# Kernel tuning notes

Measured on AMD Instinct MI355X. Metric: run time of the kernel, lower is better.

The kernel has to match this reference:

```python
import jax, jax.numpy as jnp
import numpy as np


def lstm_cell(x, h, c, Wi, Wh, b):
    # PyTorch LSTMCell gate order: i, f, g, o
    g = x @ Wi.T + h @ Wh.T + b
    i, f, gg, o = jnp.split(g, 4, axis=-1)
    c = jax.nn.sigmoid(f) * c + jax.nn.sigmoid(i) * jnp.tanh(gg)
    h = jax.nn.sigmoid(o) * jnp.tanh(c)
    return h, c


def setup_inputs() -> dict:
    key = jax.random.key(0)
    ks = jax.random.split(key, 32)
    S, B, L, N, T = 20, 16, 30, 6, 20
    H, E, Vs, Vt = 512, 512, 50000, 30000
    w = lambda k, shape: jax.random.normal(k, shape, jnp.float32) * 0.05
    return {
        'articles': jax.random.randint(ks[0], (S, B, L), 0, Vs, jnp.int32),
        'summaries': jax.random.randint(ks[1], (N, B, T), 0, Vt, jnp.int32),
        'emb_src': w(ks[2], (Vs, E)),
        'emb_tgt': w(ks[3], (Vt, E)),
        'we_Wi': w(ks[4], (4 * H, E)), 'we_Wh': w(ks[5], (4 * H, H)), 'we_b': w(ks[6], (4 * H,)),
        'se_Wi': w(ks[7], (4 * H, H)), 'se_Wh': w(ks[8], (4 * H, H)), 'se_b': w(ks[9], (4 * H,)),
        'W_feat': w(ks[10], (H, H)), 'b_feat': w(ks[11], (H,)),
        'wd_Wi': w(ks[12], (4 * H, E)), 'wd_Wh': w(ks[13], (4 * H, H)), 'wd_b': w(ks[14], (4 * H,)),
        'W_vocab': w(ks[15], (Vt, H)), 'b_vocab': w(ks[16], (Vt,)),
        'sd_Wi': w(ks[17], (4 * H, H)), 'sd_Wh': w(ks[18], (4 * H, H)), 'sd_b': w(ks[19], (4 * H,)),
        'attn_Wh': w(ks[20], (H, H)), 'attn_wc': w(ks[21], (H,)), 'attn_v': w(ks[22], (H,)),
        'W_out': w(ks[23], (H, 2 * H)), 'b_out': w(ks[24], (H,)),
    }


def _forward(articles, summaries, emb_src, emb_tgt, we_Wi, we_Wh, we_b,
             se_Wi, se_Wh, se_b, W_feat, b_feat, wd_Wi, wd_Wh, wd_b,
             W_vocab, b_vocab, sd_Wi, sd_Wh, sd_b, attn_Wh, attn_wc, attn_v,
             W_out, b_out):
    S, B, L = articles.shape
    H = we_Wh.shape[1]

    # ---- word encoder: LSTMCell over each sentence, vmapped over S ----
    def encode_sentence(tokens):  # [B, L]
        x = emb_src[tokens]  # [B, L, E]
        z = jnp.zeros((B, H), x.dtype)
        def step(hc, xt):
            h, c = lstm_cell(xt, hc[0], hc[1], we_Wi, we_Wh, we_b)
            return (h, c), None
        (h, _), _ = jax.lax.scan(step, (z, z), jnp.swapaxes(x, 0, 1))
        return h
    word_hx = jax.vmap(encode_sentence)(articles)  # [S, B, H]

    # ---- sentence encoder: LSTM over sentence dim ----
    z = jnp.zeros((B, H), word_hx.dtype)
    def senc_step(hc, x):
        h, c = lstm_cell(x, hc[0], hc[1], se_Wi, se_Wh, se_b)
        return (h, c), h
    (s_hx, s_cx), sent_out = jax.lax.scan(senc_step, (z, z), word_hx)  # sent_out [S,B,H]
    sent_feat = sent_out @ W_feat.T + b_feat  # precomputed attention features

    mask = (articles[:, :, 0:1] > 0).astype(jnp.float32)  # [S, B, 1]
    coverage0 = jnp.zeros_like(mask)

    # ---- hierarchical decoder over summary sentences ----
    def sent_step(carry, sent):  # sent [B, T]
        w_hx, w_cx, s_hx, s_cx, coverage, loss = carry
        seq = sent.T  # [T, B]

        def word_step(wc, ba):
            wh, wcell, l = wc
            wb, wa = ba
            wh, wcell = lstm_cell(emb_tgt[wb], wh, wcell, wd_Wi, wd_Wh, wd_b)
            logits = wh @ W_vocab.T + b_vocab  # [B, V]
            logp = jax.nn.log_softmax(logits, axis=-1)
            nll = -jnp.take_along_axis(logp, wa[:, None], axis=1)[:, 0]
            m = (wa != 0).astype(logits.dtype)  # ignore_index=0
            l = l + jnp.sum(nll * m) / jnp.maximum(jnp.sum(m), 1.0)
            return (wh, wcell, l), None

        (w_hx, w_cx, loss), _ = jax.lax.scan(word_step, (w_hx, w_cx, loss), (seq[:-1], seq[1:]))

        # sentence decoder step with coverage attention over S sentences
        s_h2, s_cx = lstm_cell(w_hx, s_hx, s_cx, sd_Wi, sd_Wh, sd_b)
        e = jnp.einsum('sbh,h->sb', jnp.tanh(sent_feat + s_h2 @ attn_Wh.T + coverage * attn_wc), attn_v)
        e = jnp.where(mask[:, :, 0] > 0, e, -1e9)
        align = jax.nn.softmax(e, axis=0)[:, :, None]  # [S, B, 1]
        context = jnp.sum(align * sent_out, axis=0)  # [B, H]
        final = jnp.tanh(jnp.concatenate([context, s_h2], axis=-1) @ W_out.T + b_out)
        # coverage loss (with pre-update coverage), then accumulate coverage
        loss = loss + jnp.mean(jnp.sum(jnp.minimum(align[:, :, 0], coverage[:, :, 0]), axis=0))
        coverage = coverage + align
        return (final, w_cx, final, s_cx, coverage, loss), None

    init = (s_hx, s_cx, s_hx, s_cx, coverage0, jnp.float32(0.0))
    (_, _, _, _, _, loss), _ = jax.lax.scan(sent_step, init, summaries)
    return loss


def reference(articles, summaries, emb_src, emb_tgt, we_Wi, we_Wh, we_b,
              se_Wi, se_Wh, se_b, W_feat, b_feat, wd_Wi, wd_Wh, wd_b,
              W_vocab, b_vocab, sd_Wi, sd_Wh, sd_b, attn_Wh, attn_wc, attn_v,
              W_out, b_out):
    return _forward(articles, summaries, emb_src, emb_tgt, we_Wi, we_Wh, we_b,
                    se_Wi, se_Wh, se_b, W_feat, b_feat, wd_Wi, wd_Wh, wd_b,
                    W_vocab, b_vocab, sd_Wi, sd_Wh, sd_b, attn_Wh, attn_wc,
                    attn_v, W_out, b_out)
```

## Files before the change

kernel.cpp:

```cpp
#include <hip/hip_runtime.h>
#include <hip/hip_cooperative_groups.h>
#include <cstdint>
#include <cstddef>

namespace cg = cooperative_groups;

#define H 512
#define SS 20
#define BB 16
#define LL 30
#define NN 6
#define TT 20
#define VT 30000
#define MROWS 1824
#define NSTEPS 114
#define MPAD 1856
#define NT2 118
#define NVBLK 3422

typedef __attribute__((ext_vector_type(8))) short bf16x8;
typedef __attribute__((ext_vector_type(4))) float f32x4;

__device__ __forceinline__ float sigmoidf_(float x) { return 1.f / (1.f + expf(-x)); }
__device__ __forceinline__ float b2f(ushort u) { return __uint_as_float(((uint32_t)u) << 16); }
__device__ __forceinline__ ushort f2b_rne(float f) {
  uint32_t u = __float_as_uint(f);
  return (ushort)((u + 0x7fffu + ((u >> 16) & 1u)) >> 16);
}

struct PrepP {
  const int* articles; const int* summaries;
  const float* emb_src; const float* emb_tgt;
  const float* we_Wi; const float* wd_Wi; const float* we_Wh;
  const float* se_Wi; const float* se_Wh; const float* W_feat;
  const float* wd_Wh; const float* sd_Wi; const float* sd_Wh;
  const float* attn_Wh; const float* W_out;
  ushort* A_we; ushort* A_wd;
  ushort* weWi; ushort* wdWi; ushort* weWh;
  ushort* seWi; ushort* seWh; ushort* wfeat;
  ushort* wdWh; ushort* sdWi; ushort* sdWh;
  ushort* attnWh; ushort* Wout;
};

__device__ __forceinline__ void conv_f2b(const float* __restrict__ src,
                                         ushort* __restrict__ dst, int n4,
                                         int t0, int stride)
{
  for (int i = t0; i < n4; i += stride) {
    float4 v = reinterpret_cast<const float4*>(src)[i];
    ushort4 o;
    o.x = f2b_rne(v.x); o.y = f2b_rne(v.y);
    o.z = f2b_rne(v.z); o.w = f2b_rne(v.w);
    reinterpret_cast<ushort4*>(dst)[i] = o;
  }
}

__global__ __launch_bounds__(256) void prep_kernel(PrepP P)
{
  const int t0 = blockIdx.x * 256 + threadIdx.x;
  const int stride = gridDim.x * 256;
  for (int i = t0; i < SS * BB * LL * H; i += stride) {
    int m = i >> 9, k = i & 511;
    int l = m / (SS * BB), sb = m % (SS * BB);
    int tok = P.articles[sb * LL + l];
    P.A_we[i] = f2b_rne(P.emb_src[(size_t)tok * H + k]);
  }
  for (int i = t0; i < MROWS * H; i += stride) {
    int m = i >> 9, k = i & 511;
    int stp = m >> 4, b = m & 15;
    int n = stp / (TT - 1), t = stp % (TT - 1);
    int tok = P.summaries[(n * BB + b) * TT + t];
    P.A_wd[i] = f2b_rne(P.emb_tgt[(size_t)tok * H + k]);
  }
  const int Q = 4 * H * H / 4;
  conv_f2b(P.we_Wi, P.weWi, Q, t0, stride);
  conv_f2b(P.wd_Wi, P.wdWi, Q, t0, stride);
  conv_f2b(P.we_Wh, P.weWh, Q, t0, stride);
  conv_f2b(P.se_Wi, P.seWi, Q, t0, stride);
  conv_f2b(P.se_Wh, P.seWh, Q, t0, stride);
  conv_f2b(P.wd_Wh, P.wdWh, Q, t0, stride);
  conv_f2b(P.sd_Wi, P.sdWi, Q, t0, stride);
  conv_f2b(P.sd_Wh, P.sdWh, Q, t0, stride);
  conv_f2b(P.W_feat, P.wfeat, H * H / 4, t0, stride);
  conv_f2b(P.attn_Wh, P.attnWh, H * H / 4, t0, stride);
  conv_f2b(P.W_out, P.Wout, H * 2 * H / 4, t0, stride);
}

__global__ __launch_bounds__(512) void proj_mfma_kernel(
    const ushort* __restrict__ A_we, const ushort* __restrict__ weWi,
    const float* __restrict__ we_b, ushort* __restrict__ XiW,
    const ushort* __restrict__ A_wd, const ushort* __restrict__ wdWi,
    const float* __restrict__ wd_b, ushort* __restrict__ XiD)
{
  int bid = blockIdx.x;
  const ushort* A; const ushort* W; const float* bias; ushort* C; int M, mt, nt;
  if (bid < 1200) { A = A_we; W = weWi; bias = we_b; C = XiW; M = 9600; mt = bid >> 3; nt = bid & 7; }
  else { int b2 = bid - 1200; A = A_wd; W = wdWi; bias = wd_b; C = XiD; M = MROWS; mt = b2 >> 3; nt = b2 & 7; }
  const int tid = threadIdx.x, wid = tid >> 6, lane = tid & 63;
  const int wm = wid >> 2, wn = wid & 3;
  const int m0 = mt * 64 + wm * 32, n0 = nt * 256 + wn * 64;
  const int lr = lane & 15, lk = (lane >> 4) << 3;

  f32x4 acc[2][4];
#pragma unroll
  for (int i = 0; i < 2; ++i)
#pragma unroll
    for (int nf = 0; nf < 4; ++nf) acc[i][nf] = (f32x4)0.0f;

  for (int k0 = 0; k0 < H; k0 += 32) {
    bf16x8 a[2], b[4];
#pragma unroll
    for (int i = 0; i < 2; ++i) {
      int m = m0 + i * 16 + lr;
      bf16x8 az = (bf16x8)(short)0;
      if (m < M) az = *reinterpret_cast<const bf16x8*>(A + (size_t)m * H + k0 + lk);
      a[i] = az;
    }
#pragma unroll
    for (int nf = 0; nf < 4; ++nf)
      b[nf] = *reinterpret_cast<const bf16x8*>(W + (size_t)(n0 + nf * 16 + lr) * H + k0 + lk);
#pragma unroll
    for (int i = 0; i < 2; ++i)
#pragma unroll
      for (int nf = 0; nf < 4; ++nf)
        acc[i][nf] = __builtin_amdgcn_mfma_f32_16x16x32_bf16(a[i], b[nf], acc[i][nf], 0, 0, 0);
  }
#pragma unroll
  for (int i = 0; i < 2; ++i)
#pragma unroll
    for (int nf = 0; nf < 4; ++nf) {
      int n = n0 + nf * 16 + lr;
      float bv = bias[n];
#pragma unroll
      for (int jreg = 0; jreg < 4; ++jreg) {
        int row = m0 + i * 16 + (lane >> 4) * 4 + jreg;
        if (row < M) C[(size_t)row * 2048 + n] = f2b_rne(acc[i][nf][jreg] + bv);
      }
    }
}

struct UP {
  const ushort* XiW; const ushort* XiD;
  const ushort* weWh; const ushort* seWi; const ushort* seWh;
  const ushort* wfeat; const ushort* wdWh; const ushort* sdWi;
  const ushort* sdWh; const ushort* attnWh; const ushort* Wout;
  const float* se_b; const float* b_feat; const float* sd_b; const float* b_out;
  const float* attn_wc; const float* attn_v; const int* articles;
  ushort* h0; ushort* h1;
  float* XiS;
  ushort* sh0; ushort* sh1;
  float* sent_out;
  ushort* sent_out_bf;
  float* sent_feat;
  ushort* wh_bf;
  ushort* sdh_bf;
  ushort* final_bf;
  ushort* catb;
  float* qb;
  float* ebuf; float* alignb; float* covb; float* loss;
  const float* Wv; ushort* Wv_bf;
};

__global__ __launch_bounds__(512) void uni_kernel(UP P)
{
  cg::grid_group gg = cg::this_grid();
  const int tid = threadIdx.x, bid = blockIdx.x;
  const int wid = tid >> 6, lane = tid & 63;
  const int gw = bid * 8 + wid;
  const int lr = lane & 15;
  const int lk = (lane >> 4) << 3;
  const int orow = (lane >> 4) << 2;

  {
    float cst[5][4];
#pragma unroll
    for (int it = 0; it < 5; ++it)
#pragma unroll
      for (int rg = 0; rg < 4; ++rg) cst[it][rg] = 0.f;
    ushort* cur = P.h0;
    ushort* nxt = P.h1;
    const int ug = gw & 31;
    const int unit = ug * 16 + lr;
    const ushort* wb = P.weWh + (size_t)(ug * 16 + lr) * H + lk;
    for (int l = 0; l < LL; ++l) {
#pragma unroll
      for (int it = 0; it < 5; ++it) {
        int item = gw + it * 128;
        int mt = item >> 5;
        f32x4 acc[4];
#pragma unroll
        for (int g = 0; g < 4; ++g) acc[g] = (f32x4)0.0f;
        const ushort* ab = cur + (size_t)(mt * 16 + lr) * H + lk;
#pragma unroll
        for (int k0 = 0; k0 < H; k0 += 32) {
          bf16x8 a = *reinterpret_cast<const bf16x8*>(ab + k0);
#pragma unroll
          for (int g = 0; g < 4; ++g) {
            bf16x8 b = *reinterpret_cast<const bf16x8*>(wb + (size_t)g * H * H + k0);
            acc[g] = __builtin_amdgcn_mfma_f32_16x16x32_bf16(a, b, acc[g], 0, 0, 0);
          }
        }
#pragma unroll
        for (int rg = 0; rg < 4; ++rg) {
          int row = mt * 16 + orow + rg;
          const ushort* xi = P.XiW + (size_t)(l * 320 + row) * 2048 + unit;
          float gi = acc[0][rg] + b2f(xi[0]);
          float gf = acc[1][rg] + b2f(xi[512]);
          float gc = acc[2][rg] + b2f(xi[1024]);
          float go = acc[3][rg] + b2f(xi[1536]);
          float c = sigmoidf_(gf) * cst[it][rg] + sigmoidf_(gi) * tanhf(gc);
          float h = sigmoidf_(go) * tanhf(c);
          cst[it][rg] = c;
          nxt[(size_t)row * H + unit] = f2b_rne(h);
        }
      }
      gg.sync();
      ushort* t = cur; cur = nxt; nxt = t;
    }
    {
      const ushort* wbs = P.seWi + (size_t)(ug * 16 + lr) * H + lk;
#pragma unroll
      for (int it = 0; it < 5; ++it) {
        int item = gw + it * 128;
        int mt = item >> 5;
        f32x4 acc[4];
#pragma unroll
        for (int g = 0; g < 4; ++g) acc[g] = (f32x4)0.0f;
        const ushort* ab = cur + (size_t)(mt * 16 + lr) * H + lk;
#pragma unroll
        for (int k0 = 0; k0 < H; k0 += 32) {
          bf16x8 a = *reinterpret_cast<const bf16x8*>(ab + k0);
#pragma unroll
          for (int g = 0; g < 4; ++g) {
            bf16x8 b = *reinterpret_cast<const bf16x8*>(wbs + (size_t)g * H * H + k0);
            acc[g] = __builtin_amdgcn_mfma_f32_16x16x32_bf16(a, b, acc[g], 0, 0, 0);
          }
        }
#pragma unroll
        for (int rg = 0; rg < 4; ++rg) {
          int row = mt * 16 + orow + rg;
#pragma unroll
          for (int g = 0; g < 4; ++g)
            P.XiS[(size_t)row * 2048 + g * H + unit] = acc[g][rg] + P.se_b[g * H + unit];
        }
      }
    }
    {
      const int t0 = bid * 512 + tid;
      const int n4 = VT * H / 4;
      for (int i = t0; i < n4; i += 16 * 512) {
        float4 v = reinterpret_cast<const float4*>(P.Wv)[i];
        ushort4 o;
        o.x = f2b_rne(v.x); o.y = f2b_rne(v.y);
        o.z = f2b_rne(v.z); o.w = f2b_rne(v.w);
        reinterpret_cast<ushort4*>(P.Wv_bf)[i] = o;
      }
    }
    gg.sync();
  }

  float cw[4], csd[4];
  {
    float cse[4] = {0.f, 0.f, 0.f, 0.f};
    ushort* cur = P.sh0;
    ushort* nxt = P.sh1;
    const int ug = bid * 2 + wid;
    const int unit = ug * 16 + lr;
    for (int s = 0; s < SS; ++s) {
      if (wid < 2) {
        f32x4 acc[4];
#pragma unroll
        for (int g = 0; g < 4; ++g) acc[g] = (f32x4)0.0f;
        const ushort* ab = cur + (size_t)lr * H + lk;
        const ushort* wb = P.seWh + (size_t)(ug * 16 + lr) * H + lk;
#pragma unroll
        for (int k0 = 0; k0 < H; k0 += 32) {
          bf16x8 a = *reinterpret_cast<const bf16x8*>(ab + k0);
#pragma unroll
          for (int g = 0; g < 4; ++g) {
            bf16x8 b = *reinterpret_cast<const bf16x8*>(wb + (size_t)g * H * H + k0);
            acc[g] = __builtin_amdgcn_mfma_f32_16x16x32_bf16(a, b, acc[g], 0, 0, 0);
          }
        }
#pragma unroll
        for (int rg = 0; rg < 4; ++rg) {
          int row = orow + rg;
          const float* xi = P.XiS + (size_t)(s * 16 + row) * 2048 + unit;
          float gi = acc[0][rg] + xi[0];
          float gf = acc[1][rg] + xi[512];
          float gc = acc[2][rg] + xi[1024];
          float go = acc[3][rg] + xi[1536];
          float c = sigmoidf_(gf) * cse[rg] + sigmoidf_(gi) * tanhf(gc);
          float h = sigmoidf_(go) * tanhf(c);
          cse[rg] = c;
          nxt[(size_t)row * H + unit] = f2b_rne(h);
          P.sent_out[(size_t)(s * 16 + row) * H + unit] = h;
          P.sent_out_bf[(size_t)(s * 16 + row) * H + unit] = f2b_rne(h);
        }
      }
      gg.sync();
      ushort* t = cur; cur = nxt; nxt = t;
    }
#pragma unroll
    for (int rg = 0; rg < 4; ++rg) { cw[rg] = cse[rg]; csd[rg] = cse[rg]; }
  }

  {
    const int ug = gw & 31;
    const int unit = ug * 16 + lr;
    const ushort* wb = P.wfeat + (size_t)(ug * 16 + lr) * H + lk;
#pragma unroll
    for (int it = 0; it < 5; ++it) {
      int item = gw + it * 128;
      int mt = item >> 5;
      f32x4 acc = (f32x4)0.0f;
      const ushort* ab = P.sent_out_bf + (size_t)(mt * 16 + lr) * H + lk;
#pragma unroll
      for (int k0 = 0; k0 < H; k0 += 32) {
        bf16x8 a = *reinterpret_cast<const bf16x8*>(ab + k0);
        bf16x8 b = *reinterpret_cast<const bf16x8*>(wb + k0);
        acc = __builtin_amdgcn_mfma_f32_16x16x32_bf16(a, b, acc, 0, 0, 0);
      }
#pragma unroll
      for (int rg = 0; rg < 4; ++rg) {
        int row = mt * 16 + orow + rg;
        P.sent_feat[(size_t)row * H + unit] = acc[rg] + P.b_feat[unit];
      }
    }
    gg.sync();
  }

  {
    const int ug = bid * 2 + wid;
    const int unit = ug * 16 + lr;
    for (int n = 0; n < NN; ++n) {
      for (int t = 0; t < TT - 1; ++t) {
        int stp = n * (TT - 1) + t;
        if (wid < 2) {
          const ushort* A = (t == 0)
              ? ((n == 0) ? P.sh0 : P.final_bf)
              : P.wh_bf + (size_t)(stp - 1) * 16 * H;
          f32x4 acc[4];
#pragma unroll
          for (int g = 0; g < 4; ++g) acc[g] = (f32x4)0.0f;
          const ushort* ab = A + (size_t)lr * H + lk;
          const ushort* wb = P.wdWh + (size_t)(ug * 16 + lr) * H + lk;
#pragma unroll
          for (int k0 = 0; k0 < H; k0 += 32) {
            bf16x8 a = *reinterpret_cast<const bf16x8*>(ab + k0);
#pragma unroll
            for (int g = 0; g < 4; ++g) {
              bf16x8 b = *reinterpret_cast<const bf16x8*>(wb + (size_t)g * H * H + k0);
              acc[g] = __builtin_amdgcn_mfma_f32_16x16x32_bf16(a, b, acc[g], 0, 0, 0);
            }
          }
#pragma unroll
          for (int rg = 0; rg < 4; ++rg) {
            int row = orow + rg;
            const ushort* xi = P.XiD + (size_t)(stp * 16 + row) * 2048 + unit;
            float gi = acc[0][rg] + b2f(xi[0]);
            float gf = acc[1][rg] + b2f(xi[512]);
            float gc = acc[2][rg] + b2f(xi[1024]);
            float go = acc[3][rg] + b2f(xi[1536]);
            float c = sigmoidf_(gf) * cw[rg] + sigmoidf_(gi) * tanhf(gc);
            float h = sigmoidf_(go) * tanhf(c);
            cw[rg] = c;
            P.wh_bf[(size_t)(stp * 16 + row) * H + unit] = f2b_rne(h);
          }
        }
        gg.sync();
      }
      if (wid < 2) {
        f32x4 acc[4];
#pragma unroll
        for (int g = 0; g < 4; ++g) acc[g] = (f32x4)0.0f;
        const ushort* A1 = P.wh_bf + (size_t)(n * (TT - 1) + TT - 2) * 16 * H;
        const ushort* A2 = (n == 0) ? P.sh0 : P.final_bf;
        const ushort* ab1 = A1 + (size_t)lr * H + lk;
        const ushort* wb1 = P.sdWi + (size_t)(ug * 16 + lr) * H + lk;
#pragma unroll
        for (int k0 = 0; k0 < H; k0 += 32) {
          bf16x8 a = *reinterpret_cast<const bf16x8*>(ab1 + k0);
#pragma unroll
          for (int g = 0; g < 4; ++g) {
            bf16x8 b = *reinterpret_cast<const bf16x8*>(wb1 + (size_t)g * H * H + k0);
            acc[g] = __builtin_amdgcn_mfma_f32_16x16x32_bf16(a, b, acc[g], 0, 0, 0);
          }
        }
        const ushort* ab2 = A2 + (size_t)lr * H + lk;
        const ushort* wb2 = P.sdWh + (size_t)(ug * 16 + lr) * H + lk;
#pragma unroll
        for (int k0 = 0; k0 < H; k0 += 32) {
          bf16x8 a = *reinterpret_cast<const bf16x8*>(ab2 + k0);
#pragma unroll
          for (int g = 0; g < 4; ++g) {
            bf16x8 b = *reinterpret_cast<const bf16x8*>(wb2 + (size_t)g * H * H + k0);
            acc[g] = __builtin_amdgcn_mfma_f32_16x16x32_bf16(a, b, acc[g], 0, 0, 0);
          }
        }
#pragma unroll
        for (int rg = 0; rg < 4; ++rg) {
          int row = orow + rg;
          float gi = acc[0][rg] + P.sd_b[0 * H + unit];
          float gf = acc[1][rg] + P.sd_b[1 * H + unit];
          float gc = acc[2][rg] + P.sd_b[2 * H + unit];
          float go = acc[3][rg] + P.sd_b[3 * H + unit];
          float c = sigmoidf_(gf) * csd[rg] + sigmoidf_(gi) * tanhf(gc);
          float h = sigmoidf_(go) * tanhf(c);
          csd[rg] = c;
          P.sdh_bf[(size_t)row * H + unit] = f2b_rne(h);
        }
      }
      gg.sync();
      if (wid < 2) {
        f32x4 acc = (f32x4)0.0f;
        const ushort* ab = P.sdh_bf + (size_t)lr * H + lk;
        const ushort* wb = P.attnWh + (size_t)(ug * 16 + lr) * H + lk;
#pragma unroll
        for (int k0 = 0; k0 < H; k0 += 32) {
          bf16x8 a = *reinterpret_cast<const bf16x8*>(ab + k0);
          bf16x8 b = *reinterpret_cast<const bf16x8*>(wb + k0);
          acc = __builtin_amdgcn_mfma_f32_16x16x32_bf16(a, b, acc, 0, 0, 0);
        }
#pragma unroll
        for (int rg = 0; rg < 4; ++rg)
          P.qb[(size_t)(orow + rg) * H + unit] = acc[rg];
      }
      gg.sync();
      for (int sb = gw; sb < 320; sb += 128) {
        int b = sb & 15;
        float cov = P.covb[sb];
        float sum = 0.f;
        for (int h2 = lane; h2 < H; h2 += 64)
          sum += tanhf(P.sent_feat[(size_t)sb * H + h2] + P.qb[b * H + h2] +
                       cov * P.attn_wc[h2]) * P.attn_v[h2];
#pragma unroll
        for (int d = 1; d < 64; d <<= 1) sum += __shfl_xor(sum, d);
        if (lane == 0)
          P.ebuf[sb] = (P.articles[sb * LL] > 0) ? sum : -1e9f;
      }
      gg.sync();
      if (wid == 0 && bid < 16) {
        int b = bid;
        float ev = (lane < SS) ? P.ebuf[lane * 16 + b] : -3.0e38f;
        float mx = ev;
#pragma unroll
        for (int d = 1; d < 64; d <<= 1) mx = fmaxf(mx, __shfl_xor(mx, d));
        float ex = (lane < SS) ? expf(ev - mx) : 0.f;
        float s = ex;
#pragma unroll
        for (int d = 1; d < 64; d <<= 1) s += __shfl_xor(s, d);
        float al = ex / s;
        float cl = 0.f;
        if (lane < SS) {
          int sb = lane * 16 + b;
          float cov = P.covb[sb];
          cl = fminf(al, cov);
          P.covb[sb] = cov + al;
          P.alignb[sb] = al;
        }
#pragma unroll
        for (int d = 1; d < 64; d <<= 1) cl += __shfl_xor(cl, d);
        if (lane == 0) atomicAdd(P.loss, cl * (1.f / BB));
      }
      gg.sync();
      {
        int idx = bid * 512 + tid;
        int b = idx >> 9, h2 = idx & 511;
        float s = 0.f;
#pragma unroll
        for (int ss2 = 0; ss2 < SS; ++ss2)
          s += P.alignb[ss2 * 16 + b] * P.sent_out[(size_t)(ss2 * 16 + b) * H + h2];
        P.catb[b * 1024 + h2] = f2b_rne(s);
        P.catb[b * 1024 + 512 + h2] = P.sdh_bf[(size_t)b * H + h2];
      }
      gg.sync();
      if (wid < 2) {
        f32x4 acc = (f32x4)0.0f;
        const ushort* ab = P.catb + (size_t)lr * 1024 + lk;
        const ushort* wb = P.Wout + (size_t)(ug * 16 + lr) * 1024 + lk;
#pragma unroll
        for (int k0 = 0; k0 < 1024; k0 += 32) {
          bf16x8 a = *reinterpret_cast<const bf16x8*>(ab + k0);
          bf16x8 b = *reinterpret_cast<const bf16x8*>(wb + k0);
          acc = __builtin_amdgcn_mfma_f32_16x16x32_bf16(a, b, acc, 0, 0, 0);
        }
#pragma unroll
        for (int rg = 0; rg < 4; ++rg) {
          int row = orow + rg;
          float v = tanhf(acc[rg] + P.b_out[unit]);
          P.final_bf[(size_t)row * H + unit] = f2b_rne(v);
        }
      }
      gg.sync();
    }
  }
}

__global__ __launch_bounds__(512) void vocab_mfma_kernel(
    const ushort* __restrict__ A, const ushort* __restrict__ W,
    const float* __restrict__ bias, float* __restrict__ partials)
{
  int bid = blockIdx.x;
  const int q = NVBLK / 8, rr8 = NVBLK % 8;
  int xcd = bid & 7, idx8 = bid >> 3;
  int wid0 = (xcd < rr8) ? xcd * (q + 1) + idx8 : rr8 * (q + 1) + (xcd - rr8) * q + idx8;
  const int nt = wid0 / 29, mt = wid0 % 29;

  __shared__ float red[4][64][2];
  const int tid = threadIdx.x;
  const int wid = tid >> 6, lane = tid & 63;
  const int wm = wid >> 2, wn = wid & 3;
  const int m0 = mt * 64 + wm * 32;
  const int n0 = nt * 256 + wn * 64;
  const int lr = lane & 15;
  const int lk = (lane >> 4) << 3;

  f32x4 acc[2][4];
#pragma unroll
  for (int i = 0; i < 2; ++i)
#pragma unroll
    for (int nf = 0; nf < 4; ++nf) acc[i][nf] = (f32x4)0.0f;

  for (int k0 = 0; k0 < H; k0 += 32) {
    bf16x8 a[2], b[4];
#pragma unroll
    for (int i = 0; i < 2; ++i)
      a[i] = *reinterpret_cast<const bf16x8*>(A + (size_t)(m0 + i * 16 + lr) * H + k0 + lk);
#pragma unroll
    for (int nf = 0; nf < 4; ++nf) {
      int n = n0 + nf * 16 + lr;
      bf16x8 bz = (bf16x8)(short)0;
      if (n < VT) bz = *reinterpret_cast<const bf16x8*>(W + (size_t)n * H + k0 + lk);
      b[nf] = bz;
    }
#pragma unroll
    for (int i = 0; i < 2; ++i)
#pragma unroll
      for (int nf = 0; nf < 4; ++nf)
        acc[i][nf] = __builtin_amdgcn_mfma_f32_16x16x32_bf16(a[i], b[nf], acc[i][nf], 0, 0, 0);
  }

  float bc[4];
  int val[4];
#pragma unroll
  for (int nf = 0; nf < 4; ++nf) {
    int n = n0 + nf * 16 + lr;
    val[nf] = (n < VT);
    bc[nf] = val[nf] ? bias[n] : 0.f;
  }
#pragma unroll
  for (int i = 0; i < 2; ++i) {
#pragma unroll
    for (int jreg = 0; jreg < 4; ++jreg) {
      float lg[4];
      float mx = -3.0e38f;
#pragma unroll
      for (int nf = 0; nf < 4; ++nf) {
        lg[nf] = val[nf] ? (acc[i][nf][jreg] + bc[nf]) : -3.0e38f;
        mx = fmaxf(mx, lg[nf]);
      }
#pragma unroll
      for (int d = 1; d < 16; d <<= 1) mx = fmaxf(mx, __shfl_xor(mx, d));
      float s = 0.f;
#pragma unroll
      for (int nf = 0; nf < 4; ++nf) s += val[nf] ? expf(lg[nf] - mx) : 0.f;
#pragma unroll
      for (int d = 1; d < 16; d <<= 1) s += __shfl_xor(s, d);
      if (lr == 0) {
        int rloc = wm * 32 + i * 16 + (lane >> 4) * 4 + jreg;
        red[wn][rloc][0] = mx;
        red[wn][rloc][1] = s;
      }
    }
  }
  __syncthreads();
  if (tid < 64) {
    int r2 = tid;
    float M = -3.0e38f;
#pragma unroll
    for (int w = 0; w < 4; ++w) M = fmaxf(M, red[w][r2][0]);
    float S = 0.f;
#pragma unroll
    for (int w = 0; w < 4; ++w) S += red[w][r2][1] * expf(red[w][r2][0] - M);
    size_t p = ((size_t)(mt * 64 + r2) * NT2 + nt) * 2;
    partials[p] = M;
    partials[p + 1] = S;
  }
}

__global__ void tlog_kernel(const ushort* __restrict__ wh_bf,
                            const ushort* __restrict__ Wv_bf,
                            const float* __restrict__ bv,
                            const int* __restrict__ summaries,
                            float* __restrict__ tlog)
{
  int row = blockIdx.x;
  int lane = threadIdx.x;
  int b = row & 15, stp = row >> 4;
  int n = stp / (TT - 1), t = stp % (TT - 1);
  int tgt = summaries[(n * BB + b) * TT + t + 1];
  float s = 0.f;
  for (int k = lane; k < H; k += 64)
    s += b2f(wh_bf[(size_t)row * H + k]) * b2f(Wv_bf[(size_t)tgt * H + k]);
#pragma unroll
  for (int d = 1; d < 64; d <<= 1) s += __shfl_xor(s, d);
  if (lane == 0) tlog[row] = s + bv[tgt];
}

__global__ __launch_bounds__(256) void nll_kernel(
    const float* __restrict__ partials, const float* __restrict__ tlog,
    const int* __restrict__ summaries, float* __restrict__ loss)
{
  int stp = blockIdx.x;
  int tid = threadIdx.x;
  int rr = tid >> 4, ch = tid & 15;
  int row = stp * 16 + rr;
  const float* pr = partials + (size_t)row * NT2 * 2;
  float mx = -3.0e38f;
  for (int t2 = ch; t2 < NT2; t2 += 16) mx = fmaxf(mx, pr[t2 * 2]);
#pragma unroll
  for (int d = 1; d < 16; d <<= 1) mx = fmaxf(mx, __shfl_xor(mx, d));
  float s = 0.f;
  for (int t2 = ch; t2 < NT2; t2 += 16) s += pr[t2 * 2 + 1] * expf(pr[t2 * 2] - mx);
#pragma unroll
  for (int d = 1; d < 16; d <<= 1) s += __shfl_xor(s, d);
  __shared__ float sh_n[16], sh_m[16];
  if (ch == 0) {
    float lse = mx + logf(s);
    float nll = lse - tlog[row];
    int b = row & 15;
    int n = stp / (TT - 1), t = stp % (TT - 1);
    int wa = summaries[(n * BB + b) * TT + t + 1];
    sh_n[rr] = (wa != 0) ? nll : 0.f;
    sh_m[rr] = (wa != 0) ? 1.f : 0.f;
  }
  __syncthreads();
  if (tid == 0) {
    float sn = 0.f, sm = 0.f;
    for (int r2 = 0; r2 < 16; ++r2) { sn += sh_n[r2]; sm += sh_m[r2]; }
    atomicAdd(loss, sn / fmaxf(sm, 1.f));
  }
}

extern "C" void kernel_launch(void* const* d_in, const int* in_sizes, int n_in,
                              void* d_out, int out_size, void* d_ws, size_t ws_size,
                              hipStream_t stream)
{
  (void)in_sizes; (void)n_in; (void)out_size; (void)ws_size;
  const int*   articles  = (const int*)d_in[0];
  const int*   summaries = (const int*)d_in[1];
  const float* emb_src   = (const float*)d_in[2];
  const float* emb_tgt   = (const float*)d_in[3];
  const float* we_Wi = (const float*)d_in[4];
  const float* we_Wh = (const float*)d_in[5];
  const float* we_b  = (const float*)d_in[6];
  const float* se_Wi = (const float*)d_in[7];
  const float* se_Wh = (const float*)d_in[8];
  const float* se_b  = (const float*)d_in[9];
  const float* W_feat = (const float*)d_in[10];
  const float* b_feat = (const float*)d_in[11];
  const float* wd_Wi = (const float*)d_in[12];
  const float* wd_Wh = (const float*)d_in[13];
  const float* wd_b  = (const float*)d_in[14];
  const float* W_vocab = (const float*)d_in[15];
  const float* b_vocab = (const float*)d_in[16];
  const float* sd_Wi = (const float*)d_in[17];
  const float* sd_Wh = (const float*)d_in[18];
  const float* sd_b  = (const float*)d_in[19];
  const float* attn_Wh = (const float*)d_in[20];
  const float* attn_wc = (const float*)d_in[21];
  const float* attn_v  = (const float*)d_in[22];
  const float* W_out = (const float*)d_in[23];
  const float* b_out = (const float*)d_in[24];

  char* wsb = (char*)d_ws;
  size_t off = 0;
  auto alloc = [&](size_t bytes) -> char* {
    char* p = wsb + off;
    off += (bytes + 255) & ~(size_t)255;
    return p;
  };

  char* regA = alloc(9830400);
  ushort* A_we     = (ushort*)regA;
  ushort* wh_bf    = (ushort*)regA;
  float*  partials = (float*)(regA + 1900544);
  float*  tlogb    = (float*)(regA + 3652608);

  ushort* A_wd = (ushort*)alloc((size_t)MROWS * H * 2);

  char* regW = alloc((size_t)9600 * 2048 * 2);
  ushort* XiW   = (ushort*)regW;
  ushort* Wv_bf = (ushort*)regW;

  ushort* XiD = (ushort*)alloc((size_t)MROWS * 2048 * 2);

  ushort* weWi  = (ushort*)alloc(4 * H * H * 2);
  ushort* wdWi  = (ushort*)alloc(4 * H * H * 2);
  ushort* weWh  = (ushort*)alloc(4 * H * H * 2);
  ushort* seWi  = (ushort*)alloc(4 * H * H * 2);
  ushort* seWh  = (ushort*)alloc(4 * H * H * 2);
  ushort* wdWh  = (ushort*)alloc(4 * H * H * 2);
  ushort* sdWi  = (ushort*)alloc(4 * H * H * 2);
  ushort* sdWh  = (ushort*)alloc(4 * H * H * 2);
  ushort* wfeat = (ushort*)alloc(H * H * 2);
  ushort* attnWh= (ushort*)alloc(H * H * 2);
  ushort* Wout  = (ushort*)alloc(H * 2 * H * 2);

  float*  XiS = (float*)alloc((size_t)320 * 2048 * 4);
  ushort* h0  = (ushort*)alloc(320 * H * 2);
  ushort* h1  = (ushort*)alloc(320 * H * 2);
  ushort* sh0 = (ushort*)alloc(16 * H * 2);
  ushort* sh1 = (ushort*)alloc(16 * H * 2);
  float*  sent_out    = (float*)alloc(320 * H * 4);
  ushort* sent_out_bf = (ushort*)alloc(320 * H * 2);
  float*  sent_feat   = (float*)alloc(320 * H * 4);
  ushort* sdh_bf   = (ushort*)alloc(16 * H * 2);
  ushort* final_bf = (ushort*)alloc(16 * H * 2);
  ushort* catb     = (ushort*)alloc(16 * 1024 * 2);
  float*  qb       = (float*)alloc(16 * H * 4);
  float*  ebuf   = (float*)alloc(1280);
  float*  alignb = (float*)alloc(1280);
  float*  covb   = (float*)alloc(1280);

  float* loss = (float*)d_out;
  hipMemsetAsync(loss, 0, 4, stream);
  hipMemsetAsync(covb, 0, 1280, stream);
  hipMemsetAsync(h0, 0, 320 * H * 2, stream);
  hipMemsetAsync(sh0, 0, 16 * H * 2, stream);

  {
    PrepP P = {articles, summaries, emb_src, emb_tgt,
               we_Wi, wd_Wi, we_Wh, se_Wi, se_Wh, W_feat,
               wd_Wh, sd_Wi, sd_Wh, attn_Wh, W_out,
               A_we, A_wd, weWi, wdWi, weWh, seWi, seWh, wfeat,
               wdWh, sdWi, sdWh, attnWh, Wout};
    prep_kernel<<<2048, 256, 0, stream>>>(P);
  }

  proj_mfma_kernel<<<1432, 512, 0, stream>>>(A_we, weWi, we_b, XiW,
                                             A_wd, wdWi, wd_b, XiD);

  hipMemsetAsync((char*)wh_bf + (size_t)MROWS * H * 2, 0,
                 (size_t)(MPAD - MROWS) * H * 2, stream);

  {
    UP P;
    P.XiW = XiW; P.XiD = XiD;
    P.weWh = weWh; P.seWi = seWi; P.seWh = seWh; P.wfeat = wfeat;
    P.wdWh = wdWh; P.sdWi = sdWi; P.sdWh = sdWh; P.attnWh = attnWh; P.Wout = Wout;
    P.se_b = se_b; P.b_feat = b_feat; P.sd_b = sd_b; P.b_out = b_out;
    P.attn_wc = attn_wc; P.attn_v = attn_v; P.articles = articles;
    P.h0 = h0; P.h1 = h1; P.XiS = XiS; P.sh0 = sh0; P.sh1 = sh1;
    P.sent_out = sent_out; P.sent_out_bf = sent_out_bf; P.sent_feat = sent_feat;
    P.wh_bf = wh_bf; P.sdh_bf = sdh_bf; P.final_bf = final_bf; P.catb = catb;
    P.qb = qb; P.ebuf = ebuf; P.alignb = alignb; P.covb = covb; P.loss = loss;
    P.Wv = W_vocab; P.Wv_bf = Wv_bf;
    void* args[] = {&P};
    hipLaunchCooperativeKernel((void*)uni_kernel, dim3(16), dim3(512), args, 0, stream);
  }

  vocab_mfma_kernel<<<NVBLK, 512, 0, stream>>>(wh_bf, Wv_bf, b_vocab, partials);
  tlog_kernel<<<MROWS, 64, 0, stream>>>(wh_bf, Wv_bf, b_vocab, summaries, tlogb);
  nll_kernel<<<NSTEPS, 256, 0, stream>>>(partials, tlogb, summaries, loss);
}
```

Measured before the change: 6.011 ms.

## Replace cooperative grid sync with atomic barrier; restructure vocab GEMM and decoder recurrence

```diff
diff --git a/kernel.cpp b/kernel.cpp
--- a/kernel.cpp
+++ b/kernel.cpp
@@ -1,9 +1,6 @@
 #include <hip/hip_runtime.h>
-#include <hip/hip_cooperative_groups.h>
 #include <cstdint>
 #include <cstddef>
-
-namespace cg = cooperative_groups;
 
 #define H 512
 #define SS 20
@@ -15,8 +12,9 @@
 #define MROWS 1824
 #define NSTEPS 114
 #define MPAD 1856
-#define NT2 118
-#define NVBLK 3422
+#define NT2 120
+#define VBLK 232
+#define UBLK 16
 
 typedef __attribute__((ext_vector_type(8))) short bf16x8;
 typedef __attribute__((ext_vector_type(4))) float f32x4;
@@ -26,6 +24,23 @@
 __device__ __forceinline__ ushort f2b_rne(float f) {
   uint32_t u = __float_as_uint(f);
   return (ushort)((u + 0x7fffu + ((u >> 16) & 1u)) >> 16);
+}
+
+__device__ __forceinline__ void gbar(uint* cnt, uint* gen, uint nblk)
+{
+  __syncthreads();
+  if (threadIdx.x == 0) {
+    uint g = __hip_atomic_load(gen, __ATOMIC_RELAXED, __HIP_MEMORY_SCOPE_AGENT);
+    uint v = __hip_atomic_fetch_add(cnt, 1u, __ATOMIC_ACQ_REL, __HIP_MEMORY_SCOPE_AGENT);
+    if (v == nblk - 1u) {
+      __hip_atomic_store(cnt, 0u, __ATOMIC_RELAXED, __HIP_MEMORY_SCOPE_AGENT);
+      __hip_atomic_store(gen, g + 1u, __ATOMIC_RELEASE, __HIP_MEMORY_SCOPE_AGENT);
+    } else {
+      while (__hip_atomic_load(gen, __ATOMIC_ACQUIRE, __HIP_MEMORY_SCOPE_AGENT) == g)
+        __builtin_amdgcn_s_sleep(2);
+    }
+  }
+  __syncthreads();
 }
 
 struct PrepP {
@@ -149,21 +164,15 @@
   ushort* h0; ushort* h1;
   float* XiS;
   ushort* sh0; ushort* sh1;
-  float* sent_out;
-  ushort* sent_out_bf;
-  float* sent_feat;
-  ushort* wh_bf;
-  ushort* sdh_bf;
-  ushort* final_bf;
-  ushort* catb;
-  float* qb;
-  float* ebuf; float* alignb; float* covb; float* loss;
-  const float* Wv; ushort* Wv_bf;
+  float* sent_out; ushort* sent_out_bf; float* sent_feat;
+  ushort* wh_bf; ushort* sdh_bf; ushort* final_bf; ushort* catb;
+  float* qb; float* ebuf; float* alignb; float* covb; float* loss;
+  uint* bcnt; uint* bgen;
 };
 
 __global__ __launch_bounds__(512) void uni_kernel(UP P)
 {
-  cg::grid_group gg = cg::this_grid();
+  __shared__ f32x4 hred[2][4][64];
   const int tid = threadIdx.x, bid = blockIdx.x;
   const int wid = tid >> 6, lane = tid & 63;
   const int gw = bid * 8 + wid;
@@ -214,7 +223,7 @@
           nxt[(size_t)row * H + unit] = f2b_rne(h);
         }
       }
-      gg.sync();
+      gbar(P.bcnt, P.bgen, UBLK);
       ushort* t = cur; cur = nxt; nxt = t;
     }
     {
@@ -245,21 +254,11 @@
         }
       }
     }
-    {
-      const int t0 = bid * 512 + tid;
-      const int n4 = VT * H / 4;
-      for (int i = t0; i < n4; i += 16 * 512) {
-        float4 v = reinterpret_cast<const float4*>(P.Wv)[i];
-        ushort4 o;
-        o.x = f2b_rne(v.x); o.y = f2b_rne(v.y);
-        o.z = f2b_rne(v.z); o.w = f2b_rne(v.w);
-        reinterpret_cast<ushort4*>(P.Wv_bf)[i] = o;
-      }
-    }
-    gg.sync();
-  }
-
-  float cw[4], csd[4];
+    gbar(P.bcnt, P.bgen, UBLK);
+  }
+
+  float cw[4] = {0.f, 0.f, 0.f, 0.f};
+  float csd[4] = {0.f, 0.f, 0.f, 0.f};
   {
     float cse[4] = {0.f, 0.f, 0.f, 0.f};
     ushort* cur = P.sh0;
@@ -298,11 +297,21 @@
           P.sent_out_bf[(size_t)(s * 16 + row) * H + unit] = f2b_rne(h);
         }
       }
-      gg.sync();
+      gbar(P.bcnt, P.bgen, UBLK);
       ushort* t = cur; cur = nxt; nxt = t;
     }
-#pragma unroll
-    for (int rg = 0; rg < 4; ++rg) { cw[rg] = cse[rg]; csd[rg] = cse[rg]; }
+    if (wid < 2) {
+      f32x4 v; v[0] = cse[0]; v[1] = cse[1]; v[2] = cse[2]; v[3] = cse[3];
+      hred[wid][0][lane] = v;
+#pragma unroll
+      for (int rg = 0; rg < 4; ++rg) csd[rg] = cse[rg];
+    }
+    __syncthreads();
+    if (wid < 4 && !(wid & 1)) {
+      f32x4 v = hred[wid >> 1][0][lane];
+      cw[0] = v[0]; cw[1] = v[1]; cw[2] = v[2]; cw[3] = v[3];
+    }
+    __syncthreads();
   }
 
   {
@@ -327,37 +336,60 @@
         P.sent_feat[(size_t)row * H + unit] = acc[rg] + P.b_feat[unit];
       }
     }
-    gg.sync();
+    gbar(P.bcnt, P.bgen, UBLK);
   }
 
   {
+    const int half = wid & 1;
+    const int ug2 = bid * 2 + (wid >> 1);
+    const int unit2 = ug2 * 16 + lr;
     const int ug = bid * 2 + wid;
     const int unit = ug * 16 + lr;
+
     for (int n = 0; n < NN; ++n) {
+      bf16x8 wreg[4][8];
+      if (wid < 4) {
+#pragma unroll
+        for (int g = 0; g < 4; ++g)
+#pragma unroll
+          for (int kk = 0; kk < 8; ++kk)
+            wreg[g][kk] = *reinterpret_cast<const bf16x8*>(
+                P.wdWh + (size_t)g * H * H + (size_t)(ug2 * 16 + lr) * H +
+                half * 256 + kk * 32 + lk);
+      }
       for (int t = 0; t < TT - 1; ++t) {
         int stp = n * (TT - 1) + t;
-        if (wid < 2) {
+        f32x4 acc[4];
+        if (wid < 4) {
           const ushort* A = (t == 0)
               ? ((n == 0) ? P.sh0 : P.final_bf)
               : P.wh_bf + (size_t)(stp - 1) * 16 * H;
-          f32x4 acc[4];
 #pragma unroll
           for (int g = 0; g < 4; ++g) acc[g] = (f32x4)0.0f;
-          const ushort* ab = A + (size_t)lr * H + lk;
-          const ushort* wb = P.wdWh + (size_t)(ug * 16 + lr) * H + lk;
-#pragma unroll
-          for (int k0 = 0; k0 < H; k0 += 32) {
-            bf16x8 a = *reinterpret_cast<const bf16x8*>(ab + k0);
-#pragma unroll
-            for (int g = 0; g < 4; ++g) {
-              bf16x8 b = *reinterpret_cast<const bf16x8*>(wb + (size_t)g * H * H + k0);
-              acc[g] = __builtin_amdgcn_mfma_f32_16x16x32_bf16(a, b, acc[g], 0, 0, 0);
-            }
+          const ushort* ab = A + (size_t)lr * H + half * 256 + lk;
+#pragma unroll
+          for (int kk = 0; kk < 8; ++kk) {
+            bf16x8 a = *reinterpret_cast<const bf16x8*>(ab + kk * 32);
+#pragma unroll
+            for (int g = 0; g < 4; ++g)
+              acc[g] = __builtin_amdgcn_mfma_f32_16x16x32_bf16(a, wreg[g][kk], acc[g], 0, 0, 0);
+          }
+          if (half) {
+#pragma unroll
+            for (int g = 0; g < 4; ++g) hred[wid >> 1][g][lane] = acc[g];
+          }
+        }
+        __syncthreads();
+        if (wid < 4 && !half) {
+#pragma unroll
+          for (int g = 0; g < 4; ++g) {
+            f32x4 o = hred[wid >> 1][g][lane];
+            acc[g] += o;
           }
 #pragma unroll
           for (int rg = 0; rg < 4; ++rg) {
             int row = orow + rg;
-            const ushort* xi = P.XiD + (size_t)(stp * 16 + row) * 2048 + unit;
+            const ushort* xi = P.XiD + (size_t)(stp * 16 + row) * 2048 + unit2;
             float gi = acc[0][rg] + b2f(xi[0]);
             float gf = acc[1][rg] + b2f(xi[512]);
             float gc = acc[2][rg] + b2f(xi[1024]);
@@ -365,10 +397,10 @@
             float c = sigmoidf_(gf) * cw[rg] + sigmoidf_(gi) * tanhf(gc);
             float h = sigmoidf_(go) * tanhf(c);
             cw[rg] = c;
-            P.wh_bf[(size_t)(stp * 16 + row) * H + unit] = f2b_rne(h);
+            P.wh_bf[(size_t)(stp * 16 + row) * H + unit2] = f2b_rne(h);
           }
         }
-        gg.sync();
+        gbar(P.bcnt, P.bgen, UBLK);
       }
       if (wid < 2) {
         f32x4 acc[4];
@@ -411,7 +443,7 @@
           P.sdh_bf[(size_t)row * H + unit] = f2b_rne(h);
         }
       }
-      gg.sync();
+      gbar(P.bcnt, P.bgen, UBLK);
       if (wid < 2) {
         f32x4 acc = (f32x4)0.0f;
         const ushort* ab = P.sdh_bf + (size_t)lr * H + lk;
@@ -426,7 +458,7 @@
         for (int rg = 0; rg < 4; ++rg)
           P.qb[(size_t)(orow + rg) * H + unit] = acc[rg];
       }
-      gg.sync();
+      gbar(P.bcnt, P.bgen, UBLK);
       for (int sb = gw; sb < 320; sb += 128) {
         int b = sb & 15;
         float cov = P.covb[sb];
@@ -439,8 +471,8 @@
         if (lane == 0)
           P.ebuf[sb] = (P.articles[sb * LL] > 0) ? sum : -1e9f;
       }
-      gg.sync();
-      if (wid == 0 && bid < 16) {
+      gbar(P.bcnt, P.bgen, UBLK);
+      if (wid == 0) {
         int b = bid;
         float ev = (lane < SS) ? P.ebuf[lane * 16 + b] : -3.0e38f;
         float mx = ev;
@@ -463,7 +495,7 @@
         for (int d = 1; d < 64; d <<= 1) cl += __shfl_xor(cl, d);
         if (lane == 0) atomicAdd(P.loss, cl * (1.f / BB));
       }
-      gg.sync();
+      gbar(P.bcnt, P.bgen, UBLK);
       {
         int idx = bid * 512 + tid;
         int b = idx >> 9, h2 = idx & 511;
@@ -474,7 +506,7 @@
         P.catb[b * 1024 + h2] = f2b_rne(s);
         P.catb[b * 1024 + 512 + h2] = P.sdh_bf[(size_t)b * H + h2];
       }
-      gg.sync();
+      gbar(P.bcnt, P.bgen, UBLK);
       if (wid < 2) {
         f32x4 acc = (f32x4)0.0f;
         const ushort* ab = P.catb + (size_t)lr * 1024 + lk;
@@ -492,100 +524,119 @@
           P.final_bf[(size_t)row * H + unit] = f2b_rne(v);
         }
       }
-      gg.sync();
-    }
-  }
-}
-
-__global__ __launch_bounds__(512) void vocab_mfma_kernel(
-    const ushort* __restrict__ A, const ushort* __restrict__ W,
-    const float* __restrict__ bias, float* __restrict__ partials)
+      gbar(P.bcnt, P.bgen, UBLK);
+    }
+  }
+}
+
+__global__ __launch_bounds__(512) void vocab_kernel(
+    const ushort* __restrict__ A, const float* __restrict__ Wf,
+    ushort* __restrict__ Wbf, const float* __restrict__ bias,
+    float* __restrict__ partials, uint* bcnt, uint* bgen)
 {
-  int bid = blockIdx.x;
-  const int q = NVBLK / 8, rr8 = NVBLK % 8;
-  int xcd = bid & 7, idx8 = bid >> 3;
-  int wid0 = (xcd < rr8) ? xcd * (q + 1) + idx8 : rr8 * (q + 1) + (xcd - rr8) * q + idx8;
-  const int nt = wid0 / 29, mt = wid0 % 29;
+  {
+    int t0 = blockIdx.x * 512 + threadIdx.x;
+    const int n4 = VT * H / 4;
+    for (int i = t0; i < n4; i += VBLK * 512) {
+      float4 v = reinterpret_cast<const float4*>(Wf)[i];
+      ushort4 o;
+      o.x = f2b_rne(v.x); o.y = f2b_rne(v.y);
+      o.z = f2b_rne(v.z); o.w = f2b_rne(v.w);
+      reinterpret_cast<ushort4*>(Wbf)[i] = o;
+    }
+  }
+  gbar(bcnt, bgen, VBLK);
 
   __shared__ float red[4][64][2];
+  const int bid = blockIdx.x;
+  const int chunk = bid & 7, mt = bid >> 3;
   const int tid = threadIdx.x;
   const int wid = tid >> 6, lane = tid & 63;
   const int wm = wid >> 2, wn = wid & 3;
   const int m0 = mt * 64 + wm * 32;
-  const int n0 = nt * 256 + wn * 64;
   const int lr = lane & 15;
   const int lk = (lane >> 4) << 3;
 
-  f32x4 acc[2][4];
+  bf16x8 areg[2][16];
 #pragma unroll
   for (int i = 0; i < 2; ++i)
 #pragma unroll
-    for (int nf = 0; nf < 4; ++nf) acc[i][nf] = (f32x4)0.0f;
-
-  for (int k0 = 0; k0 < H; k0 += 32) {
-    bf16x8 a[2], b[4];
+    for (int kk = 0; kk < 16; ++kk)
+      areg[i][kk] = *reinterpret_cast<const bf16x8*>(
+          A + (size_t)(m0 + i * 16 + lr) * H + kk * 32 + lk);
+
+  for (int nt2 = 0; nt2 < 15; ++nt2) {
+    const int n0 = chunk * 3840 + nt2 * 256 + wn * 64;
+    f32x4 acc[2][4];
 #pragma unroll
     for (int i = 0; i < 2; ++i)
-      a[i] = *reinterpret_cast<const bf16x8*>(A + (size_t)(m0 + i * 16 + lr) * H + k0 + lk);
+#pragma unroll
+      for (int nf = 0; nf < 4; ++nf) acc[i][nf] = (f32x4)0.0f;
+
+#pragma unroll 4
+    for (int kk = 0; kk < 16; ++kk) {
+      bf16x8 b[4];
+#pragma unroll
+      for (int nf = 0; nf < 4; ++nf) {
+        int n = n0 + nf * 16 + lr;
+        bf16x8 bz = (bf16x8)(short)0;
+        if (n < VT) bz = *reinterpret_cast<const bf16x8*>(Wbf + (size_t)n * H + kk * 32 + lk);
+        b[nf] = bz;
+      }
+#pragma unroll
+      for (int i = 0; i < 2; ++i)
+#pragma unroll
+        for (int nf = 0; nf < 4; ++nf)
+          acc[i][nf] = __builtin_amdgcn_mfma_f32_16x16x32_bf16(areg[i][kk], b[nf], acc[i][nf], 0, 0, 0);
+    }
+
+    float bc[4];
+    int val[4];
 #pragma unroll
     for (int nf = 0; nf < 4; ++nf) {
       int n = n0 + nf * 16 + lr;
-      bf16x8 bz = (bf16x8)(short)0;
-      if (n < VT) bz = *reinterpret_cast<const bf16x8*>(W + (size_t)n * H + k0 + lk);
-      b[nf] = bz;
-    }
-#pragma unroll
-    for (int i = 0; i < 2; ++i)
-#pragma unroll
-      for (int nf = 0; nf < 4; ++nf)
-        acc[i][nf] = __builtin_amdgcn_mfma_f32_16x16x32_bf16(a[i], b[nf], acc[i][nf], 0, 0, 0);
-  }
-
-  float bc[4];
-  int val[4];
-#pragma unroll
-  for (int nf = 0; nf < 4; ++nf) {
-    int n = n0 + nf * 16 + lr;
-    val[nf] = (n < VT);
-    bc[nf] = val[nf] ? bias[n] : 0.f;
-  }
-#pragma unroll
-  for (int i = 0; i < 2; ++i) {
-#pragma unroll
-    for (int jreg = 0; jreg < 4; ++jreg) {
-      float lg[4];
-      float mx = -3.0e38f;
-#pragma unroll
-      for (int nf = 0; nf < 4; ++nf) {
-        lg[nf] = val[nf] ? (acc[i][nf][jreg] + bc[nf]) : -3.0e38f;
-        mx = fmaxf(mx, lg[nf]);
-      }
-#pragma unroll
-      for (int d = 1; d < 16; d <<= 1) mx = fmaxf(mx, __shfl_xor(mx, d));
-      float s = 0.f;
-#pragma unroll
-      for (int nf = 0; nf < 4; ++nf) s += val[nf] ? expf(lg[nf] - mx) : 0.f;
-#pragma unroll
-      for (int d = 1; d < 16; d <<= 1) s += __shfl_xor(s, d);
-      if (lr == 0) {
-        int rloc = wm * 32 + i * 16 + (lane >> 4) * 4 + jreg;
-        red[wn][rloc][0] = mx;
-        red[wn][rloc][1] = s;
-      }
-    }
-  }
-  __syncthreads();
-  if (tid < 64) {
-    int r2 = tid;
-    float M = -3.0e38f;
-#pragma unroll
-    for (int w = 0; w < 4; ++w) M = fmaxf(M, red[w][r2][0]);
-    float S = 0.f;
-#pragma unroll
-    for (int w = 0; w < 4; ++w) S += red[w][r2][1] * expf(red[w][r2][0] - M);
-    size_t p = ((size_t)(mt * 64 + r2) * NT2 + nt) * 2;
-    partials[p] = M;
-    partials[p + 1] = S;
+      val[nf] = (n < VT);
+      bc[nf] = val[nf] ? bias[n] : 0.f;
+    }
+#pragma unroll
+    for (int i = 0; i < 2; ++i) {
+#pragma unroll
+      for (int jreg = 0; jreg < 4; ++jreg) {
+        float lg[4];
+        float mx = -3.0e38f;
+#pragma unroll
+        for (int nf = 0; nf < 4; ++nf) {
+          lg[nf] = val[nf] ? (acc[i][nf][jreg] + bc[nf]) : -3.0e38f;
+          mx = fmaxf(mx, lg[nf]);
+        }
+#pragma unroll
+        for (int d = 1; d < 16; d <<= 1) mx = fmaxf(mx, __shfl_xor(mx, d));
+        float s = 0.f;
+#pragma unroll
+        for (int nf = 0; nf < 4; ++nf) s += val[nf] ? expf(lg[nf] - mx) : 0.f;
+#pragma unroll
+        for (int d = 1; d < 16; d <<= 1) s += __shfl_xor(s, d);
+        if (lr == 0) {
+          int rloc = wm * 32 + i * 16 + (lane >> 4) * 4 + jreg;
+          red[wn][rloc][0] = mx;
+          red[wn][rloc][1] = s;
+        }
+      }
+    }
+    __syncthreads();
+    if (tid < 64) {
+      int r2 = tid;
+      float M = -3.0e38f;
+#pragma unroll
+      for (int w = 0; w < 4; ++w) M = fmaxf(M, red[w][r2][0]);
+      float S = 0.f;
+#pragma unroll
+      for (int w = 0; w < 4; ++w) S += red[w][r2][1] * expf(red[w][r2][0] - M);
+      size_t p = ((size_t)(mt * 64 + r2) * NT2 + chunk * 15 + nt2) * 2;
+      partials[p] = M;
+      partials[p + 1] = S;
+    }
+    __syncthreads();
   }
 }
 
@@ -686,7 +737,7 @@
   ushort* A_we     = (ushort*)regA;
   ushort* wh_bf    = (ushort*)regA;
   float*  partials = (float*)(regA + 1900544);
-  float*  tlogb    = (float*)(regA + 3652608);
+  float*  tlogb    = (float*)(regA + 3682304);
 
   ushort* A_wd = (ushort*)alloc((size_t)MROWS * H * 2);
 
@@ -723,12 +774,14 @@
   float*  ebuf   = (float*)alloc(1280);
   float*  alignb = (float*)alloc(1280);
   float*  covb   = (float*)alloc(1280);
+  uint*   bar    = (uint*)alloc(256);
 
   float* loss = (float*)d_out;
   hipMemsetAsync(loss, 0, 4, stream);
   hipMemsetAsync(covb, 0, 1280, stream);
   hipMemsetAsync(h0, 0, 320 * H * 2, stream);
   hipMemsetAsync(sh0, 0, 16 * H * 2, stream);
+  hipMemsetAsync(bar, 0, 256, stream);
 
   {
     PrepP P = {articles, summaries, emb_src, emb_tgt,
@@ -756,12 +809,12 @@
     P.sent_out = sent_out; P.sent_out_bf = sent_out_bf; P.sent_feat = sent_feat;
     P.wh_bf = wh_bf; P.sdh_bf = sdh_bf; P.final_bf = final_bf; P.catb = catb;
     P.qb = qb; P.ebuf = ebuf; P.alignb = alignb; P.covb = covb; P.loss = loss;
-    P.Wv = W_vocab; P.Wv_bf = Wv_bf;
-    void* args[] = {&P};
-    hipLaunchCooperativeKernel((void*)uni_kernel, dim3(16), dim3(512), args, 0, stream);
-  }
-
-  vocab_mfma_kernel<<<NVBLK, 512, 0, stream>>>(wh_bf, Wv_bf, b_vocab, partials);
+    P.bcnt = bar; P.bgen = bar + 1;
+    uni_kernel<<<UBLK, 512, 0, stream>>>(P);
+  }
+
+  vocab_kernel<<<VBLK, 512, 0, stream>>>(wh_bf, W_vocab, Wv_bf, b_vocab,
+                                         partials, bar + 2, bar + 3);
   tlog_kernel<<<MROWS, 64, 0, stream>>>(wh_bf, Wv_bf, b_vocab, summaries, tlogb);
   nll_kernel<<<NSTEPS, 256, 0, stream>>>(partials, tlogb, summaries, loss);
 }
```

Result: faster. 5.198 ms (-13.5%).
